# Kernel optimization log

Hardware: AMD Instinct MI355X
Metric: run time of the kernel (lower is better)

## Reference

```python
import jax, jax.numpy as jnp
import numpy as np

N = 200000          # graph_size (stalk rows)
H = 128             # hidden_channels
NNZ = 3200000       # Laplacian nnz (avg degree 16)
K = 15              # polynomial degree (poly_layers_K)
LAMBDA_MAX = 2.0    # normalised Laplacian -> analytic lambda_max


def setup_inputs() -> dict:
    key = jax.random.key(0)
    ks = jax.random.split(key, 6)
    x = jax.random.normal(ks[0], (N, H), dtype=jnp.float32)
    vals = jax.random.normal(ks[1], (NNZ,), dtype=jnp.float32)
    poly_logits = jax.random.normal(ks[2], (K + 1,), dtype=jnp.float32)
    hp_alpha = jax.random.normal(ks[3], (), dtype=jnp.float32)
    edge_row = jax.random.randint(ks[4], (NNZ,), 0, N, dtype=jnp.int64)
    edge_col = jax.random.randint(ks[5], (NNZ,), 0, N, dtype=jnp.int64)
    return {"x": x, "vals": vals, "poly_logits": poly_logits,
            "hp_alpha": hp_alpha, "edge_row": edge_row, "edge_col": edge_col}


def reference(x, vals, poly_logits, hp_alpha, edge_row, edge_col):
    n = x.shape[0]

    def spmm(v):  # (n,h) -> (n,h), sparse L @ v in COO form
        return jax.ops.segment_sum(vals[:, None] * v[edge_col], edge_row,
                                   num_segments=n)

    def Lhat(v):  # L_hat = (2/lambda_max) L - I
        return (2.0 / LAMBDA_MAX) * spmm(v) - v

    w = jax.nn.softmax(poly_logits)  # mixture over Chebyshev T_0..T_K

    # Chebyshev Type-1 recurrence: T_{k+1} = 2 L_hat T_k - T_{k-1}
    T0 = x
    T1 = Lhat(x)
    out = w[0] * T0 + w[1] * T1

    def step(carry, wk):
        T0, T1, out = carry
        Tk1 = 2.0 * Lhat(T1) - T0
        return (T1, Tk1, out + wk * Tk1), None

    (_, _, px), _ = jax.lax.scan(step, (T0, T1, out), w[2:])

    # high-pass term: x - (1/lambda_max) L x
    hp = x - spmm(x) / LAMBDA_MAX
    return -px + hp_alpha * hp
```

## Files before the change

### kernel.cpp

```cpp
#include <hip/hip_runtime.h>
#include <math.h>

#define N_NODES 200000
#define H_CH    128
#define GRP     64
#define NNZ_E   3200000
#define K_DEG   15

#define EPB     4096
#define BSHIFT  9
#define BROWS   512
#define NBUCK   391
#define BCAP    9216

__global__ void softmax_k(const float* __restrict__ logits, float* __restrict__ w) {
    if (threadIdx.x == 0) {
        float m = -1e30f;
        for (int i = 0; i <= K_DEG; ++i) m = fmaxf(m, logits[i]);
        float e[K_DEG + 1];
        float s = 0.f;
        for (int i = 0; i <= K_DEG; ++i) { e[i] = expf(logits[i] - m); s += e[i]; }
        float inv = 1.0f / s;
        for (int i = 0; i <= K_DEG; ++i) w[i] = e[i] * inv;
    }
}

__global__ __launch_bounds__(256) void bucketA_k(
    const int* __restrict__ row, const int* __restrict__ col,
    const float* __restrict__ vals,
    int* __restrict__ gfill, uint2* __restrict__ stag, int nnz) {
    __shared__ int cnt[NBUCK];
    __shared__ int excl[NBUCK];
    __shared__ int gbase[NBUCK];
    __shared__ int sm[256];
    __shared__ uint2 sstag[EPB];
    __shared__ unsigned short sb[EPB];

    int tid = threadIdx.x;
    int base = blockIdx.x * EPB;

    for (int t = tid; t < NBUCK; t += 256) cnt[t] = 0;
    __syncthreads();

    int r[16], c[16], b[16];
    float v[16];
#pragma unroll
    for (int j = 0; j < 16; ++j) {
        int i = base + j * 256 + tid;
        if (i < nnz) {
            r[j] = row[i]; c[j] = col[i]; v[j] = vals[i];
            b[j] = r[j] >> BSHIFT;
            atomicAdd(&cnt[b[j]], 1);
        } else {
            b[j] = -1;
        }
    }
    __syncthreads();

    {
        int b0 = 2 * tid, b1 = 2 * tid + 1;
        int c0 = (b0 < NBUCK) ? cnt[b0] : 0;
        int c1 = (b1 < NBUCK) ? cnt[b1] : 0;
        int pair = c0 + c1;
        sm[tid] = pair;
        __syncthreads();
        int incl = pair;
        for (int off = 1; off < 256; off <<= 1) {
            int tv = (tid >= off) ? sm[tid - off] : 0;
            __syncthreads();
            incl += tv;
            sm[tid] = incl;
            __syncthreads();
        }
        int pexcl = incl - pair;
        if (b0 < NBUCK) excl[b0] = pexcl;
        if (b1 < NBUCK) excl[b1] = pexcl + c0;
    }
    __syncthreads();

    for (int t = tid; t < NBUCK; t += 256) {
        int cb = cnt[t];
        gbase[t] = (cb > 0) ? atomicAdd(&gfill[t], cb) : 0;
    }
    __syncthreads();
    for (int t = tid; t < NBUCK; t += 256) cnt[t] = excl[t];
    __syncthreads();

#pragma unroll
    for (int j = 0; j < 16; ++j) {
        if (b[j] >= 0) {
            int p = atomicAdd(&cnt[b[j]], 1);
            sstag[p] = make_uint2(((unsigned)(r[j] & 511) << 18) | (unsigned)c[j],
                                  __float_as_uint(v[j]));
            sb[p] = (unsigned short)b[j];
        }
    }
    __syncthreads();

    int tot = nnz - base; if (tot > EPB) tot = EPB;
    for (int i = tid; i < tot; i += 256) {
        int bb = sb[i];
        size_t gp = (size_t)bb * BCAP + gbase[bb] + (i - excl[bb]);
        stag[gp] = sstag[i];
    }
}

__global__ void scanG_k(const int* __restrict__ gfill, int* __restrict__ bbase,
                        int* __restrict__ row_ptr) {
    __shared__ int sm[256];
    int tid = threadIdx.x;
    int j0 = 2 * tid, j1 = 2 * tid + 1;
    int c0 = (j0 < NBUCK) ? gfill[j0] : 0;
    int c1 = (j1 < NBUCK) ? gfill[j1] : 0;
    int pair = c0 + c1;
    sm[tid] = pair;
    __syncthreads();
    int incl = pair;
    for (int off = 1; off < 256; off <<= 1) {
        int t = (tid >= off) ? sm[tid - off] : 0;
        __syncthreads();
        incl += t;
        sm[tid] = incl;
        __syncthreads();
    }
    int pexcl = incl - pair;
    if (j0 < NBUCK) bbase[j0] = pexcl;
    if (j1 < NBUCK) bbase[j1] = pexcl + c0;
    if (tid == 0) row_ptr[N_NODES] = NNZ_E;
}

__global__ __launch_bounds__(256) void bucketB_k(
    const uint2* __restrict__ stag, const int* __restrict__ gfill,
    const int* __restrict__ bbase, int* __restrict__ row_ptr,
    int2* __restrict__ csr) {
    __shared__ int hist[BROWS];
    __shared__ int lexcl[BROWS];
    __shared__ int sm[256];
    int b = blockIdx.x;
    int n = gfill[b];
    int cs = bbase[b];
    const uint2* s = stag + (size_t)b * BCAP;
    int tid = threadIdx.x;

    hist[tid] = 0; hist[tid + 256] = 0;
    __syncthreads();
    for (int i = tid; i < n; i += 256)
        atomicAdd(&hist[s[i].x >> 18], 1);
    __syncthreads();

    int j0 = 2 * tid, j1 = 2 * tid + 1;
    int c0 = hist[j0], c1 = hist[j1];
    int pair = c0 + c1;
    sm[tid] = pair;
    __syncthreads();
    int incl = pair;
    for (int off = 1; off < 256; off <<= 1) {
        int t = (tid >= off) ? sm[tid - off] : 0;
        __syncthreads();
        incl += t;
        sm[tid] = incl;
        __syncthreads();
    }
    int pexcl = incl - pair;
    lexcl[j0] = pexcl;
    lexcl[j1] = pexcl + c0;

    int rbase = b << BSHIFT;
    if (rbase + j0 < N_NODES) row_ptr[rbase + j0] = cs + lexcl[j0];
    if (rbase + j1 < N_NODES) row_ptr[rbase + j1] = cs + lexcl[j1];
    hist[j0] = lexcl[j0];
    hist[j1] = lexcl[j1];
    __syncthreads();

    for (int i = tid; i < n; i += 256) {
        uint2 e = s[i];
        int rl = (int)(e.x >> 18);
        int p = cs + atomicAdd(&hist[rl], 1);
        int2 cv;
        cv.x = (int)(e.x & 0x3FFFF);
        cv.y = (int)e.y;
        csr[p] = cv;
    }
}

__global__ __launch_bounds__(512) void first_k(
    const int* __restrict__ rp, const int2* __restrict__ csr,
    const float* __restrict__ x, float* __restrict__ T1g, float* __restrict__ out,
    const float* __restrict__ w, const float* __restrict__ alpha_p, int goff) {
    int wid = blockIdx.x * 8 + (threadIdx.x >> 6);
    int r = __builtin_amdgcn_readfirstlane(wid);
    if (r >= N_NODES) return;
    int lane = threadIdx.x & 63;
    const float* base = x + goff + lane;
    int e0 = rp[r], e1 = rp[r + 1];
    float a0 = 0.f, a1 = 0.f, a2 = 0.f, a3 = 0.f;
    float a4 = 0.f, a5 = 0.f, a6 = 0.f, a7 = 0.f;
    int e = e0;
    for (; e + 8 <= e1; e += 8) {
        int2 cv0 = csr[e],     cv1 = csr[e + 1], cv2 = csr[e + 2], cv3 = csr[e + 3];
        int2 cv4 = csr[e + 4], cv5 = csr[e + 5], cv6 = csr[e + 6], cv7 = csr[e + 7];
        a0 = fmaf(__int_as_float(cv0.y), base[(unsigned)cv0.x * H_CH], a0);
        a1 = fmaf(__int_as_float(cv1.y), base[(unsigned)cv1.x * H_CH], a1);
        a2 = fmaf(__int_as_float(cv2.y), base[(unsigned)cv2.x * H_CH], a2);
        a3 = fmaf(__int_as_float(cv3.y), base[(unsigned)cv3.x * H_CH], a3);
        a4 = fmaf(__int_as_float(cv4.y), base[(unsigned)cv4.x * H_CH], a4);
        a5 = fmaf(__int_as_float(cv5.y), base[(unsigned)cv5.x * H_CH], a5);
        a6 = fmaf(__int_as_float(cv6.y), base[(unsigned)cv6.x * H_CH], a6);
        a7 = fmaf(__int_as_float(cv7.y), base[(unsigned)cv7.x * H_CH], a7);
    }
    for (; e + 4 <= e1; e += 4) {
        int2 cv0 = csr[e], cv1 = csr[e + 1], cv2 = csr[e + 2], cv3 = csr[e + 3];
        a0 = fmaf(__int_as_float(cv0.y), base[(unsigned)cv0.x * H_CH], a0);
        a1 = fmaf(__int_as_float(cv1.y), base[(unsigned)cv1.x * H_CH], a1);
        a2 = fmaf(__int_as_float(cv2.y), base[(unsigned)cv2.x * H_CH], a2);
        a3 = fmaf(__int_as_float(cv3.y), base[(unsigned)cv3.x * H_CH], a3);
    }
    for (; e < e1; ++e) {
        int2 cv = csr[e];
        a0 = fmaf(__int_as_float(cv.y), base[(unsigned)cv.x * H_CH], a0);
    }
    float s = ((a0 + a1) + (a2 + a3)) + ((a4 + a5) + (a6 + a7));
    size_t idxg = (size_t)r * GRP + lane;
    size_t idxf = (size_t)r * H_CH + goff + lane;
    float xr = x[idxf];
    float w0 = w[0], w1 = w[1], al = alpha_p[0];
    float t1 = s - xr;
    float o = -(w0 * xr + w1 * t1) + al * (xr - 0.5f * s);
    T1g[idxg] = t1;
    out[idxf] = o;
}

__global__ __launch_bounds__(512) void cheb_k(
    const int* __restrict__ rp, const int2* __restrict__ csr,
    const float* __restrict__ Tcur, const float* TprevBase, int tprevStride,
    float* Tnext, float* __restrict__ out,
    const float* __restrict__ w, int k, int goff) {
    int wid = blockIdx.x * 8 + (threadIdx.x >> 6);
    int r = __builtin_amdgcn_readfirstlane(wid);
    if (r >= N_NODES) return;
    int lane = threadIdx.x & 63;
    const float* base = Tcur + lane;
    int e0 = rp[r], e1 = rp[r + 1];
    float a0 = 0.f, a1 = 0.f, a2 = 0.f, a3 = 0.f;
    float a4 = 0.f, a5 = 0.f, a6 = 0.f, a7 = 0.f;
    int e = e0;
    for (; e + 8 <= e1; e += 8) {
        int2 cv0 = csr[e],     cv1 = csr[e + 1], cv2 = csr[e + 2], cv3 = csr[e + 3];
        int2 cv4 = csr[e + 4], cv5 = csr[e + 5], cv6 = csr[e + 6], cv7 = csr[e + 7];
        a0 = fmaf(__int_as_float(cv0.y), base[(unsigned)cv0.x * GRP], a0);
        a1 = fmaf(__int_as_float(cv1.y), base[(unsigned)cv1.x * GRP], a1);
        a2 = fmaf(__int_as_float(cv2.y), base[(unsigned)cv2.x * GRP], a2);
        a3 = fmaf(__int_as_float(cv3.y), base[(unsigned)cv3.x * GRP], a3);
        a4 = fmaf(__int_as_float(cv4.y), base[(unsigned)cv4.x * GRP], a4);
        a5 = fmaf(__int_as_float(cv5.y), base[(unsigned)cv5.x * GRP], a5);
        a6 = fmaf(__int_as_float(cv6.y), base[(unsigned)cv6.x * GRP], a6);
        a7 = fmaf(__int_as_float(cv7.y), base[(unsigned)cv7.x * GRP], a7);
    }
    for (; e + 4 <= e1; e += 4) {
        int2 cv0 = csr[e], cv1 = csr[e + 1], cv2 = csr[e + 2], cv3 = csr[e + 3];
        a0 = fmaf(__int_as_float(cv0.y), base[(unsigned)cv0.x * GRP], a0);
        a1 = fmaf(__int_as_float(cv1.y), base[(unsigned)cv1.x * GRP], a1);
        a2 = fmaf(__int_as_float(cv2.y), base[(unsigned)cv2.x * GRP], a2);
        a3 = fmaf(__int_as_float(cv3.y), base[(unsigned)cv3.x * GRP], a3);
    }
    for (; e < e1; ++e) {
        int2 cv = csr[e];
        a0 = fmaf(__int_as_float(cv.y), base[(unsigned)cv.x * GRP], a0);
    }
    float s = ((a0 + a1) + (a2 + a3)) + ((a4 + a5) + (a6 + a7));
    size_t idxg = (size_t)r * GRP + lane;
    size_t idxf = (size_t)r * H_CH + goff + lane;
    float tc = Tcur[idxg];
    float tp = TprevBase[(size_t)r * tprevStride + lane];
    float wk = w[k];
    float tn = 2.0f * (s - tc) - tp;
    float o = out[idxf];
    o -= wk * tn;
    out[idxf] = o;
    Tnext[idxg] = tn;
}

extern "C" void kernel_launch(void* const* d_in, const int* in_sizes, int n_in,
                              void* d_out, int out_size, void* d_ws, size_t ws_size,
                              hipStream_t stream) {
    const float* x      = (const float*)d_in[0];
    const float* vals   = (const float*)d_in[1];
    const float* logits = (const float*)d_in[2];
    const float* alpha  = (const float*)d_in[3];
    const int*   erow   = (const int*)d_in[4];
    const int*   ecol   = (const int*)d_in[5];
    float* out = (float*)d_out;

    const size_t NG = (size_t)N_NODES * GRP;
    float* bufA    = (float*)d_ws;
    float* bufB    = bufA + NG;
    int2*  csr     = (int2*)(bufB + NG);
    uint2* stag    = (uint2*)(csr + NNZ_E);
    int*   row_ptr = (int*)(stag + (size_t)NBUCK * BCAP);
    int*   gfill   = row_ptr + (N_NODES + 1);
    int*   bbase   = gfill + NBUCK;
    float* w_buf   = (float*)(bbase + NBUCK);

    hipMemsetAsync(gfill, 0, NBUCK * sizeof(int), stream);
    softmax_k<<<1, 64, 0, stream>>>(logits, w_buf);

    int nblkA = (NNZ_E + EPB - 1) / EPB;
    bucketA_k<<<nblkA, 256, 0, stream>>>(erow, ecol, vals, gfill, stag, NNZ_E);
    scanG_k<<<1, 256, 0, stream>>>(gfill, bbase, row_ptr);
    bucketB_k<<<NBUCK, 256, 0, stream>>>(stag, gfill, bbase, row_ptr, csr);

    int grid = (N_NODES + 7) / 8;

    for (int g = 0; g < H_CH / GRP; ++g) {
        int goff = g * GRP;
        first_k<<<grid, 512, 0, stream>>>(row_ptr, csr, x, bufB, out, w_buf, alpha, goff);
        cheb_k<<<grid, 512, 0, stream>>>(row_ptr, csr, bufB, x + goff, H_CH, bufA,
                                         out, w_buf, 2, goff);
        float* Tcur = bufA;
        float* Tprev = bufB;
        for (int k = 3; k <= K_DEG; ++k) {
            cheb_k<<<grid, 512, 0, stream>>>(row_ptr, csr, Tcur, Tprev, GRP, Tprev,
                                             out, w_buf, k, goff);
            float* t = Tcur; Tcur = Tprev; Tprev = t;
        }
    }
}
```

Baseline: 4.393 ms.

## Process both channel halves in one pass with interleaved block scheduling

Adds a combined path where each Chebyshev step handles all 128 channels in one launch. Adjacent block groups are assigned to the same rows for the two 64-channel halves, so each row's CSR entries are read once per step instead of twice, and the number of launches is halved. Temporaries become full width, and the staging buffer is aliased onto the T buffers to save workspace. The per-group fallback kernels also lose their 8-way unroll. The combined path runs only if the workspace is large enough, and full-width T buffers cost more memory footprint and cache.

```diff
diff --git a/kernel.cpp b/kernel.cpp
--- a/kernel.cpp
+++ b/kernel.cpp
@@ -183,15 +183,19 @@
     }
 }
 
-__global__ __launch_bounds__(512) void first_k(
+
+__global__ __launch_bounds__(512) void firstC_k(
     const int* __restrict__ rp, const int2* __restrict__ csr,
-    const float* __restrict__ x, float* __restrict__ T1g, float* __restrict__ out,
-    const float* __restrict__ w, const float* __restrict__ alpha_p, int goff) {
-    int wid = blockIdx.x * 8 + (threadIdx.x >> 6);
+    const float* __restrict__ x, float* __restrict__ T1, float* __restrict__ out,
+    const float* __restrict__ w, const float* __restrict__ alpha_p) {
+    int bid = blockIdx.x;
+    int pos = (bid >> 3) * 4 + (bid & 3);
+    int wid = pos * 8 + (threadIdx.x >> 6);
     int r = __builtin_amdgcn_readfirstlane(wid);
     if (r >= N_NODES) return;
-    int lane = threadIdx.x & 63;
-    const float* base = x + goff + lane;
+    int g = (bid >> 2) & 1;
+    int ch = (g << 6) | (threadIdx.x & 63);
+    const float* base = x + ch;
     int e0 = rp[r], e1 = rp[r + 1];
     float a0 = 0.f, a1 = 0.f, a2 = 0.f, a3 = 0.f;
     float a4 = 0.f, a5 = 0.f, a6 = 0.f, a7 = 0.f;
@@ -220,6 +224,91 @@
         a0 = fmaf(__int_as_float(cv.y), base[(unsigned)cv.x * H_CH], a0);
     }
     float s = ((a0 + a1) + (a2 + a3)) + ((a4 + a5) + (a6 + a7));
+    size_t idx = (size_t)r * H_CH + ch;
+    float xr = x[idx];
+    float w0 = w[0], w1 = w[1], al = alpha_p[0];
+    float t1 = s - xr;
+    float o = -(w0 * xr + w1 * t1) + al * (xr - 0.5f * s);
+    T1[idx] = t1;
+    out[idx] = o;
+}
+
+__global__ __launch_bounds__(512) void chebC_k(
+    const int* __restrict__ rp, const int2* __restrict__ csr,
+    const float* __restrict__ Tcur, const float* __restrict__ Tprev,
+    float* __restrict__ Tnext, float* __restrict__ out,
+    const float* __restrict__ w, int k) {
+    int bid = blockIdx.x;
+    int pos = (bid >> 3) * 4 + (bid & 3);
+    int wid = pos * 8 + (threadIdx.x >> 6);
+    int r = __builtin_amdgcn_readfirstlane(wid);
+    if (r >= N_NODES) return;
+    int g = (bid >> 2) & 1;
+    int ch = (g << 6) | (threadIdx.x & 63);
+    const float* base = Tcur + ch;
+    int e0 = rp[r], e1 = rp[r + 1];
+    float a0 = 0.f, a1 = 0.f, a2 = 0.f, a3 = 0.f;
+    float a4 = 0.f, a5 = 0.f, a6 = 0.f, a7 = 0.f;
+    int e = e0;
+    for (; e + 8 <= e1; e += 8) {
+        int2 cv0 = csr[e],     cv1 = csr[e + 1], cv2 = csr[e + 2], cv3 = csr[e + 3];
+        int2 cv4 = csr[e + 4], cv5 = csr[e + 5], cv6 = csr[e + 6], cv7 = csr[e + 7];
+        a0 = fmaf(__int_as_float(cv0.y), base[(unsigned)cv0.x * H_CH], a0);
+        a1 = fmaf(__int_as_float(cv1.y), base[(unsigned)cv1.x * H_CH], a1);
+        a2 = fmaf(__int_as_float(cv2.y), base[(unsigned)cv2.x * H_CH], a2);
+        a3 = fmaf(__int_as_float(cv3.y), base[(unsigned)cv3.x * H_CH], a3);
+        a4 = fmaf(__int_as_float(cv4.y), base[(unsigned)cv4.x * H_CH], a4);
+        a5 = fmaf(__int_as_float(cv5.y), base[(unsigned)cv5.x * H_CH], a5);
+        a6 = fmaf(__int_as_float(cv6.y), base[(unsigned)cv6.x * H_CH], a6);
+        a7 = fmaf(__int_as_float(cv7.y), base[(unsigned)cv7.x * H_CH], a7);
+    }
+    for (; e + 4 <= e1; e += 4) {
+        int2 cv0 = csr[e], cv1 = csr[e + 1], cv2 = csr[e + 2], cv3 = csr[e + 3];
+        a0 = fmaf(__int_as_float(cv0.y), base[(unsigned)cv0.x * H_CH], a0);
+        a1 = fmaf(__int_as_float(cv1.y), base[(unsigned)cv1.x * H_CH], a1);
+        a2 = fmaf(__int_as_float(cv2.y), base[(unsigned)cv2.x * H_CH], a2);
+        a3 = fmaf(__int_as_float(cv3.y), base[(unsigned)cv3.x * H_CH], a3);
+    }
+    for (; e < e1; ++e) {
+        int2 cv = csr[e];
+        a0 = fmaf(__int_as_float(cv.y), base[(unsigned)cv.x * H_CH], a0);
+    }
+    float s = ((a0 + a1) + (a2 + a3)) + ((a4 + a5) + (a6 + a7));
+    size_t idx = (size_t)r * H_CH + ch;
+    float tc = Tcur[idx];
+    float tp = Tprev[idx];
+    float wk = w[k];
+    float tn = 2.0f * (s - tc) - tp;
+    float o = out[idx];
+    o -= wk * tn;
+    out[idx] = o;
+    Tnext[idx] = tn;
+}
+
+__global__ __launch_bounds__(512) void first_k(
+    const int* __restrict__ rp, const int2* __restrict__ csr,
+    const float* __restrict__ x, float* __restrict__ T1g, float* __restrict__ out,
+    const float* __restrict__ w, const float* __restrict__ alpha_p, int goff) {
+    int wid = blockIdx.x * 8 + (threadIdx.x >> 6);
+    int r = __builtin_amdgcn_readfirstlane(wid);
+    if (r >= N_NODES) return;
+    int lane = threadIdx.x & 63;
+    const float* base = x + goff + lane;
+    int e0 = rp[r], e1 = rp[r + 1];
+    float a0 = 0.f, a1 = 0.f, a2 = 0.f, a3 = 0.f;
+    int e = e0;
+    for (; e + 4 <= e1; e += 4) {
+        int2 cv0 = csr[e], cv1 = csr[e + 1], cv2 = csr[e + 2], cv3 = csr[e + 3];
+        a0 = fmaf(__int_as_float(cv0.y), base[(unsigned)cv0.x * H_CH], a0);
+        a1 = fmaf(__int_as_float(cv1.y), base[(unsigned)cv1.x * H_CH], a1);
+        a2 = fmaf(__int_as_float(cv2.y), base[(unsigned)cv2.x * H_CH], a2);
+        a3 = fmaf(__int_as_float(cv3.y), base[(unsigned)cv3.x * H_CH], a3);
+    }
+    for (; e < e1; ++e) {
+        int2 cv = csr[e];
+        a0 = fmaf(__int_as_float(cv.y), base[(unsigned)cv.x * H_CH], a0);
+    }
+    float s = (a0 + a1) + (a2 + a3);
     size_t idxg = (size_t)r * GRP + lane;
     size_t idxf = (size_t)r * H_CH + goff + lane;
     float xr = x[idxf];
@@ -242,20 +331,7 @@
     const float* base = Tcur + lane;
     int e0 = rp[r], e1 = rp[r + 1];
     float a0 = 0.f, a1 = 0.f, a2 = 0.f, a3 = 0.f;
-    float a4 = 0.f, a5 = 0.f, a6 = 0.f, a7 = 0.f;
     int e = e0;
-    for (; e + 8 <= e1; e += 8) {
-        int2 cv0 = csr[e],     cv1 = csr[e + 1], cv2 = csr[e + 2], cv3 = csr[e + 3];
-        int2 cv4 = csr[e + 4], cv5 = csr[e + 5], cv6 = csr[e + 6], cv7 = csr[e + 7];
-        a0 = fmaf(__int_as_float(cv0.y), base[(unsigned)cv0.x * GRP], a0);
-        a1 = fmaf(__int_as_float(cv1.y), base[(unsigned)cv1.x * GRP], a1);
-        a2 = fmaf(__int_as_float(cv2.y), base[(unsigned)cv2.x * GRP], a2);
-        a3 = fmaf(__int_as_float(cv3.y), base[(unsigned)cv3.x * GRP], a3);
-        a4 = fmaf(__int_as_float(cv4.y), base[(unsigned)cv4.x * GRP], a4);
-        a5 = fmaf(__int_as_float(cv5.y), base[(unsigned)cv5.x * GRP], a5);
-        a6 = fmaf(__int_as_float(cv6.y), base[(unsigned)cv6.x * GRP], a6);
-        a7 = fmaf(__int_as_float(cv7.y), base[(unsigned)cv7.x * GRP], a7);
-    }
     for (; e + 4 <= e1; e += 4) {
         int2 cv0 = csr[e], cv1 = csr[e + 1], cv2 = csr[e + 2], cv3 = csr[e + 3];
         a0 = fmaf(__int_as_float(cv0.y), base[(unsigned)cv0.x * GRP], a0);
@@ -267,7 +343,7 @@
         int2 cv = csr[e];
         a0 = fmaf(__int_as_float(cv.y), base[(unsigned)cv.x * GRP], a0);
     }
-    float s = ((a0 + a1) + (a2 + a3)) + ((a4 + a5) + (a6 + a7));
+    float s = (a0 + a1) + (a2 + a3);
     size_t idxg = (size_t)r * GRP + lane;
     size_t idxf = (size_t)r * H_CH + goff + lane;
     float tc = Tcur[idxg];
@@ -291,12 +367,19 @@
     const int*   ecol   = (const int*)d_in[5];
     float* out = (float*)d_out;
 
-    const size_t NG = (size_t)N_NODES * GRP;
+    const size_t NG  = (size_t)N_NODES * GRP;
+    const size_t NF  = (size_t)N_NODES * H_CH;
+    const size_t REQ_COMBINED =
+        (2 * NF + 0) * sizeof(float) + (size_t)NNZ_E * sizeof(int2) +
+        (N_NODES + 1 + 2 * NBUCK + 64) * sizeof(int);
+    bool combined = ws_size >= REQ_COMBINED;
+
+    const size_t TSZ = combined ? NF : NG;
     float* bufA    = (float*)d_ws;
-    float* bufB    = bufA + NG;
-    int2*  csr     = (int2*)(bufB + NG);
-    uint2* stag    = (uint2*)(csr + NNZ_E);
-    int*   row_ptr = (int*)(stag + (size_t)NBUCK * BCAP);
+    float* bufB    = bufA + TSZ;
+    int2*  csr     = (int2*)(bufB + TSZ);
+    uint2* stag    = (uint2*)bufA;
+    int*   row_ptr = (int*)(csr + NNZ_E);
     int*   gfill   = row_ptr + (N_NODES + 1);
     int*   bbase   = gfill + NBUCK;
     float* w_buf   = (float*)(bbase + NBUCK);
@@ -309,19 +392,31 @@
     scanG_k<<<1, 256, 0, stream>>>(gfill, bbase, row_ptr);
     bucketB_k<<<NBUCK, 256, 0, stream>>>(stag, gfill, bbase, row_ptr, csr);
 
-    int grid = (N_NODES + 7) / 8;
-
-    for (int g = 0; g < H_CH / GRP; ++g) {
-        int goff = g * GRP;
-        first_k<<<grid, 512, 0, stream>>>(row_ptr, csr, x, bufB, out, w_buf, alpha, goff);
-        cheb_k<<<grid, 512, 0, stream>>>(row_ptr, csr, bufB, x + goff, H_CH, bufA,
-                                         out, w_buf, 2, goff);
+    if (combined) {
+        int gridC = 2 * ((N_NODES + 7) / 8);
+        firstC_k<<<gridC, 512, 0, stream>>>(row_ptr, csr, x, bufB, out, w_buf, alpha);
+        chebC_k<<<gridC, 512, 0, stream>>>(row_ptr, csr, bufB, x, bufA, out, w_buf, 2);
         float* Tcur = bufA;
         float* Tprev = bufB;
         for (int k = 3; k <= K_DEG; ++k) {
-            cheb_k<<<grid, 512, 0, stream>>>(row_ptr, csr, Tcur, Tprev, GRP, Tprev,
-                                             out, w_buf, k, goff);
+            chebC_k<<<gridC, 512, 0, stream>>>(row_ptr, csr, Tcur, Tprev, Tprev,
+                                               out, w_buf, k);
             float* t = Tcur; Tcur = Tprev; Tprev = t;
         }
-    }
-}
+    } else {
+        int grid = (N_NODES + 7) / 8;
+        for (int g = 0; g < H_CH / GRP; ++g) {
+            int goff = g * GRP;
+            first_k<<<grid, 512, 0, stream>>>(row_ptr, csr, x, bufB, out, w_buf, alpha, goff);
+            cheb_k<<<grid, 512, 0, stream>>>(row_ptr, csr, bufB, x + goff, H_CH, bufA,
+                                             out, w_buf, 2, goff);
+            float* Tcur = bufA;
+            float* Tprev = bufB;
+            for (int k = 3; k <= K_DEG; ++k) {
+                cheb_k<<<grid, 512, 0, stream>>>(row_ptr, csr, Tcur, Tprev, GRP, Tprev,
+                                                 out, w_buf, k, goff);
+                float* t = Tcur; Tcur = Tprev; Tprev = t;
+            }
+        }
+    }
+}
```

Result: no change. 4.423 ms (+0.7%).

## Column-chunk CSR rows and process several rows per wave in Chebyshev SpMM

Applied to the files above, without the earlier changes.

The CSR build now sorts each row's edges into 7 column chunks and stores per-row chunk offsets. The Chebyshev kernel assigns 25 rows to each wave and sweeps chunk by chunk, so concurrently running waves gather from the same column range of T. The goal is to keep gathers within a cache-sized window instead of scattering across the whole vector. The output accumulation is also folded so it only runs on odd k, combining two terms and halving read-modify-write traffic on out. The staging buffer is aliased onto bufA to save workspace. The risks are a serial, dependent per-row inner loop and far fewer waves, which could expose gather latency.

```diff
diff --git a/kernel.cpp b/kernel.cpp
--- a/kernel.cpp
+++ b/kernel.cpp
@@ -12,6 +12,11 @@
 #define BROWS   512
 #define NBUCK   391
 #define BCAP    9216
+
+#define NCH     7
+
+#define CBLK    1000
+#define RPWV    25
 
 __global__ void softmax_k(const float* __restrict__ logits, float* __restrict__ w) {
     if (threadIdx.x == 0) {
@@ -132,9 +137,9 @@
 __global__ __launch_bounds__(256) void bucketB_k(
     const uint2* __restrict__ stag, const int* __restrict__ gfill,
     const int* __restrict__ bbase, int* __restrict__ row_ptr,
-    int2* __restrict__ csr) {
-    __shared__ int hist[BROWS];
-    __shared__ int lexcl[BROWS];
+    int* __restrict__ rcb, int2* __restrict__ csr) {
+    __shared__ int hist[BROWS * 8];
+    __shared__ int lexcl[BROWS * 8];
     __shared__ int sm[256];
     int b = blockIdx.x;
     int n = gfill[b];
@@ -142,18 +147,24 @@
     const uint2* s = stag + (size_t)b * BCAP;
     int tid = threadIdx.x;
 
-    hist[tid] = 0; hist[tid + 256] = 0;
-    __syncthreads();
-    for (int i = tid; i < n; i += 256)
-        atomicAdd(&hist[s[i].x >> 18], 1);
-    __syncthreads();
-
-    int j0 = 2 * tid, j1 = 2 * tid + 1;
-    int c0 = hist[j0], c1 = hist[j1];
-    int pair = c0 + c1;
-    sm[tid] = pair;
-    __syncthreads();
-    int incl = pair;
+    for (int t = tid; t < BROWS * 8; t += 256) hist[t] = 0;
+    __syncthreads();
+    for (int i = tid; i < n; i += 256) {
+        unsigned key = s[i].x;
+        int rl = (int)(key >> 18);
+        int c = (int)((key & 0x3FFFF) >> 15);
+        atomicAdd(&hist[(rl << 3) | c], 1);
+    }
+    __syncthreads();
+
+    int base16 = tid * 16;
+    int vloc[16];
+    int tsum = 0;
+#pragma unroll
+    for (int q = 0; q < 16; ++q) { vloc[q] = tsum; tsum += hist[base16 + q]; }
+    sm[tid] = tsum;
+    __syncthreads();
+    int incl = tsum;
     for (int off = 1; off < 256; off <<= 1) {
         int t = (tid >= off) ? sm[tid - off] : 0;
         __syncthreads();
@@ -161,23 +172,32 @@
         sm[tid] = incl;
         __syncthreads();
     }
-    int pexcl = incl - pair;
-    lexcl[j0] = pexcl;
-    lexcl[j1] = pexcl + c0;
+    int texcl = incl - tsum;
+#pragma unroll
+    for (int q = 0; q < 16; ++q) lexcl[base16 + q] = texcl + vloc[q];
+    __syncthreads();
 
     int rbase = b << BSHIFT;
-    if (rbase + j0 < N_NODES) row_ptr[rbase + j0] = cs + lexcl[j0];
-    if (rbase + j1 < N_NODES) row_ptr[rbase + j1] = cs + lexcl[j1];
-    hist[j0] = lexcl[j0];
-    hist[j1] = lexcl[j1];
+    for (int rl = tid; rl < BROWS; rl += 256) {
+        int r = rbase + rl;
+        if (r < N_NODES) {
+            row_ptr[r] = cs + lexcl[rl << 3];
+#pragma unroll
+            for (int c2 = 0; c2 < 8; ++c2)
+                rcb[(size_t)r * 8 + c2] = cs + lexcl[(rl << 3) | c2];
+        }
+    }
+    for (int t = tid; t < BROWS * 8; t += 256) hist[t] = lexcl[t];
     __syncthreads();
 
     for (int i = tid; i < n; i += 256) {
         uint2 e = s[i];
         int rl = (int)(e.x >> 18);
-        int p = cs + atomicAdd(&hist[rl], 1);
+        unsigned col = e.x & 0x3FFFF;
+        int c = (int)(col >> 15);
+        int p = cs + atomicAdd(&hist[(rl << 3) | c], 1);
         int2 cv;
-        cv.x = (int)(e.x & 0x3FFFF);
+        cv.x = (int)col;
         cv.y = (int)e.y;
         csr[p] = cv;
     }
@@ -230,54 +250,49 @@
     out[idxf] = o;
 }
 
-__global__ __launch_bounds__(512) void cheb_k(
-    const int* __restrict__ rp, const int2* __restrict__ csr,
+__global__ __launch_bounds__(512, 8) void chebG_k(
+    const int* __restrict__ rcb, const int2* __restrict__ csr,
     const float* __restrict__ Tcur, const float* TprevBase, int tprevStride,
     float* Tnext, float* __restrict__ out,
     const float* __restrict__ w, int k, int goff) {
-    int wid = blockIdx.x * 8 + (threadIdx.x >> 6);
-    int r = __builtin_amdgcn_readfirstlane(wid);
-    if (r >= N_NODES) return;
+    int wv = blockIdx.x * 8 + (threadIdx.x >> 6);
+    int r0 = __builtin_amdgcn_readfirstlane(wv) * RPWV;
     int lane = threadIdx.x & 63;
     const float* base = Tcur + lane;
-    int e0 = rp[r], e1 = rp[r + 1];
-    float a0 = 0.f, a1 = 0.f, a2 = 0.f, a3 = 0.f;
-    float a4 = 0.f, a5 = 0.f, a6 = 0.f, a7 = 0.f;
-    int e = e0;
-    for (; e + 8 <= e1; e += 8) {
-        int2 cv0 = csr[e],     cv1 = csr[e + 1], cv2 = csr[e + 2], cv3 = csr[e + 3];
-        int2 cv4 = csr[e + 4], cv5 = csr[e + 5], cv6 = csr[e + 6], cv7 = csr[e + 7];
-        a0 = fmaf(__int_as_float(cv0.y), base[(unsigned)cv0.x * GRP], a0);
-        a1 = fmaf(__int_as_float(cv1.y), base[(unsigned)cv1.x * GRP], a1);
-        a2 = fmaf(__int_as_float(cv2.y), base[(unsigned)cv2.x * GRP], a2);
-        a3 = fmaf(__int_as_float(cv3.y), base[(unsigned)cv3.x * GRP], a3);
-        a4 = fmaf(__int_as_float(cv4.y), base[(unsigned)cv4.x * GRP], a4);
-        a5 = fmaf(__int_as_float(cv5.y), base[(unsigned)cv5.x * GRP], a5);
-        a6 = fmaf(__int_as_float(cv6.y), base[(unsigned)cv6.x * GRP], a6);
-        a7 = fmaf(__int_as_float(cv7.y), base[(unsigned)cv7.x * GRP], a7);
-    }
-    for (; e + 4 <= e1; e += 4) {
-        int2 cv0 = csr[e], cv1 = csr[e + 1], cv2 = csr[e + 2], cv3 = csr[e + 3];
-        a0 = fmaf(__int_as_float(cv0.y), base[(unsigned)cv0.x * GRP], a0);
-        a1 = fmaf(__int_as_float(cv1.y), base[(unsigned)cv1.x * GRP], a1);
-        a2 = fmaf(__int_as_float(cv2.y), base[(unsigned)cv2.x * GRP], a2);
-        a3 = fmaf(__int_as_float(cv3.y), base[(unsigned)cv3.x * GRP], a3);
-    }
-    for (; e < e1; ++e) {
-        int2 cv = csr[e];
-        a0 = fmaf(__int_as_float(cv.y), base[(unsigned)cv.x * GRP], a0);
-    }
-    float s = ((a0 + a1) + (a2 + a3)) + ((a4 + a5) + (a6 + a7));
-    size_t idxg = (size_t)r * GRP + lane;
-    size_t idxf = (size_t)r * H_CH + goff + lane;
-    float tc = Tcur[idxg];
-    float tp = TprevBase[(size_t)r * tprevStride + lane];
-    float wk = w[k];
-    float tn = 2.0f * (s - tc) - tp;
-    float o = out[idxf];
-    o -= wk * tn;
-    out[idxf] = o;
-    Tnext[idxg] = tn;
+
+    float acc[RPWV];
+#pragma unroll
+    for (int j = 0; j < RPWV; ++j) acc[j] = 0.f;
+
+    for (int c = 0; c < NCH; ++c) {
+#pragma unroll
+        for (int j = 0; j < RPWV; ++j) {
+            const int* rb = rcb + (size_t)(r0 + j) * 8 + c;
+            int e0 = rb[0], e1 = rb[1];
+            float a = acc[j];
+            for (int e = e0; e < e1; ++e) {
+                int2 cv = csr[e];
+                a = fmaf(__int_as_float(cv.y), base[(unsigned)cv.x * GRP], a);
+            }
+            acc[j] = a;
+        }
+    }
+
+    float wk = w[k], wkm1 = w[k - 1];
+    bool doOut = (k & 1) != 0;
+#pragma unroll
+    for (int j = 0; j < RPWV; ++j) {
+        int r = r0 + j;
+        size_t idxg = (size_t)r * GRP + lane;
+        float tc = Tcur[idxg];
+        float tp = TprevBase[(size_t)r * tprevStride + lane];
+        float tn = 2.0f * (acc[j] - tc) - tp;
+        Tnext[idxg] = tn;
+        if (doOut) {
+            size_t idxf = (size_t)r * H_CH + goff + lane;
+            out[idxf] -= wkm1 * tc + wk * tn;
+        }
+    }
 }
 
 extern "C" void kernel_launch(void* const* d_in, const int* in_sizes, int n_in,
@@ -295,9 +310,10 @@
     float* bufA    = (float*)d_ws;
     float* bufB    = bufA + NG;
     int2*  csr     = (int2*)(bufB + NG);
-    uint2* stag    = (uint2*)(csr + NNZ_E);
-    int*   row_ptr = (int*)(stag + (size_t)NBUCK * BCAP);
-    int*   gfill   = row_ptr + (N_NODES + 1);
+    uint2* stag    = (uint2*)bufA;
+    int*   row_ptr = (int*)(csr + NNZ_E);
+    int*   rcb     = row_ptr + (N_NODES + 1);
+    int*   gfill   = rcb + (size_t)N_NODES * 8;
     int*   bbase   = gfill + NBUCK;
     float* w_buf   = (float*)(bbase + NBUCK);
 
@@ -307,20 +323,20 @@
     int nblkA = (NNZ_E + EPB - 1) / EPB;
     bucketA_k<<<nblkA, 256, 0, stream>>>(erow, ecol, vals, gfill, stag, NNZ_E);
     scanG_k<<<1, 256, 0, stream>>>(gfill, bbase, row_ptr);
-    bucketB_k<<<NBUCK, 256, 0, stream>>>(stag, gfill, bbase, row_ptr, csr);
-
-    int grid = (N_NODES + 7) / 8;
+    bucketB_k<<<NBUCK, 256, 0, stream>>>(stag, gfill, bbase, row_ptr, rcb, csr);
+
+    int gridF = (N_NODES + 7) / 8;
 
     for (int g = 0; g < H_CH / GRP; ++g) {
         int goff = g * GRP;
-        first_k<<<grid, 512, 0, stream>>>(row_ptr, csr, x, bufB, out, w_buf, alpha, goff);
-        cheb_k<<<grid, 512, 0, stream>>>(row_ptr, csr, bufB, x + goff, H_CH, bufA,
-                                         out, w_buf, 2, goff);
+        first_k<<<gridF, 512, 0, stream>>>(row_ptr, csr, x, bufB, out, w_buf, alpha, goff);
+        chebG_k<<<CBLK, 512, 0, stream>>>(rcb, csr, bufB, x + goff, H_CH, bufA,
+                                          out, w_buf, 2, goff);
         float* Tcur = bufA;
         float* Tprev = bufB;
         for (int k = 3; k <= K_DEG; ++k) {
-            cheb_k<<<grid, 512, 0, stream>>>(row_ptr, csr, Tcur, Tprev, GRP, Tprev,
-                                             out, w_buf, k, goff);
+            chebG_k<<<CBLK, 512, 0, stream>>>(rcb, csr, Tcur, Tprev, GRP, Tprev,
+                                              out, w_buf, k, goff);
             float* t = Tcur; Tcur = Tprev; Tprev = t;
         }
     }
```

Result: slower. 7.271 ms (+65.5%).
